# Optimization experiments

Hardware: AMD Instinct MI355X
Metric: run time of the kernel (lower is better)

Reference implementation:

```python
import jax, jax.numpy as jnp
import numpy as np

D_MODEL = 128
D_STATE = 16
D_CONV = 2
EXPAND = 2
D_INNER = EXPAND * D_MODEL  # 256
DT_RANK = (D_MODEL + 15) // 16  # 8
GROUPS = 4
EPS = 1e-5


def setup_inputs() -> dict:
    key = jax.random.key(0)
    ks = jax.random.split(key, 12)
    s = lambda k, shape, sc=0.02: jax.random.normal(k, shape, dtype=jnp.float32) * sc
    inp = {
        "x_hsi": jax.random.normal(ks[0], (8, D_MODEL, 64, 64), dtype=jnp.float32),
        "W_in": s(ks[1], (D_MODEL, 2 * D_INNER)),            # in_proj (no bias)
        "conv_w": s(ks[2], (D_INNER, D_CONV), 0.5),          # depthwise causal conv, k=2
        "conv_b": s(ks[3], (D_INNER,), 0.1),
        "W_x": s(ks[4], (D_INNER, DT_RANK + 2 * D_STATE)),   # x_proj (no bias)
        "W_dt": s(ks[5], (DT_RANK, D_INNER), 0.1),
        "b_dt": s(ks[6], (D_INNER,), 0.1),
        "A_log": jnp.log(jnp.broadcast_to(jnp.arange(1, D_STATE + 1, dtype=jnp.float32), (D_INNER, D_STATE))),
        "D": jnp.ones((D_INNER,), dtype=jnp.float32),
        "W_out": s(ks[7], (D_INNER, D_MODEL)),               # out_proj (no bias)
        "gn_gamma": jnp.ones((D_MODEL,), dtype=jnp.float32),
        "gn_beta": jnp.zeros((D_MODEL,), dtype=jnp.float32),
    }
    return inp


def _causal_conv_k2(x, w, b):
    # x: [B, L, Din]; w: [Din, 2]; causal depthwise conv, kernel size 2
    xp = jnp.pad(x, ((0, 0), (1, 0), (0, 0)))
    return xp[:, :-1] * w[:, 0] + xp[:, 1:] * w[:, 1] + b


def _selective_scan(xc, dt, Bmat, Cmat, A, D):
    # xc,dt: [B,L,Din]; Bmat,Cmat: [B,L,N]; A: [Din,N]; D: [Din]
    def step(h, inp):
        dt_t, B_t, C_t, x_t = inp          # [B,Din],[B,N],[B,N],[B,Din]
        dA = jnp.exp(dt_t[..., None] * A)                      # [B,Din,N]
        dBx = dt_t[..., None] * B_t[:, None, :] * x_t[..., None]
        h = dA * h + dBx
        y = jnp.einsum('bdn,bn->bd', h, C_t)
        return h, y

    B_, L, Din = xc.shape
    h0 = jnp.zeros((B_, Din, A.shape[1]), dtype=xc.dtype)
    xs = (jnp.swapaxes(dt, 0, 1), jnp.swapaxes(Bmat, 0, 1),
          jnp.swapaxes(Cmat, 0, 1), jnp.swapaxes(xc, 0, 1))
    _, ys = jax.lax.scan(step, h0, xs)     # ys: [L,B,Din]
    return jnp.swapaxes(ys, 0, 1) + xc * D


def _mamba(x, W_in, conv_w, conv_b, W_x, W_dt, b_dt, A_log, D, W_out):
    # x: [B, L, d_model]
    xz = x @ W_in                                   # [B,L,2*Din]
    xh, z = jnp.split(xz, 2, axis=-1)
    xh = jax.nn.silu(_causal_conv_k2(xh, conv_w, conv_b))
    x_dbl = xh @ W_x                                # [B,L,dt_rank+2N]
    dt_low = x_dbl[..., :DT_RANK]
    Bmat = x_dbl[..., DT_RANK:DT_RANK + D_STATE]
    Cmat = x_dbl[..., DT_RANK + D_STATE:]
    dt = jax.nn.softplus(dt_low @ W_dt + b_dt)      # [B,L,Din]
    A = -jnp.exp(A_log)
    y = _selective_scan(xh, dt, Bmat, Cmat, A, D)
    y = y * jax.nn.silu(z)
    return y @ W_out


def _group_norm(x, gamma, beta):
    # x: [B,C,H,W]
    B_, C, H, W = x.shape
    xr = x.reshape(B_, GROUPS, -1)
    mean = xr.mean(-1, keepdims=True)
    var = xr.var(-1, keepdims=True)
    xn = ((xr - mean) * jax.lax.rsqrt(var + EPS)).reshape(B_, C, H, W)
    return xn * gamma[:, None, None] + beta[:, None, None]


def reference(x_hsi, W_in, conv_w, conv_b, W_x, W_dt, b_dt, A_log, D, W_out, gn_gamma, gn_beta):
    B_, C, H, W = x_hsi.shape
    x = jnp.transpose(x_hsi, (0, 2, 3, 1)).reshape(B_, H * W, C)
    x = _mamba(x, W_in, conv_w, conv_b, W_x, W_dt, b_dt, A_log, D, W_out)
    x = jnp.transpose(x.reshape(B_, H, W, C), (0, 3, 1, 2))
    x = jax.nn.silu(_group_norm(x, gn_gamma, gn_beta))
    return x + x_hsi
```

## Files before the change

kernel.cpp:

```cpp
#include <hip/hip_runtime.h>
#include <hip/hip_bf16.h>
#include <hip/hip_fp16.h>
#include <math.h>

#define BATCH   8
#define LSEQ    4096
#define CMODEL  128
#define DIN     256
#define NSTATE  16
#define RRANK   8
#define NCH     128
#define TCH     32

typedef __attribute__((ext_vector_type(8))) short short8;
typedef __attribute__((ext_vector_type(4))) float f32x4;
typedef __attribute__((ext_vector_type(2))) float f32x2;

__device__ __forceinline__ float sigmoid_fast(float x) {
    return __builtin_amdgcn_rcpf(1.0f + __expf(-x));
}
__device__ __forceinline__ float silu_fast(float x) { return x * sigmoid_fast(x); }
__device__ __forceinline__ float softplus_fast(float x) {
    return fmaxf(x, 0.0f) + __logf(1.0f + __expf(-fabsf(x)));
}
__device__ __forceinline__ float bf2f(unsigned short u) {
    return __uint_as_float(((unsigned)u) << 16);
}
__device__ __forceinline__ unsigned pk2bf(float a, float b) {
    __hip_bfloat162 t = __float22bfloat162_rn(make_float2(a, b));
    unsigned r;
    __builtin_memcpy(&r, &t, 4);
    return r;
}
__device__ __forceinline__ unsigned short f2bf1(float v) {
    return (unsigned short)pk2bf(v, v);
}

__device__ __forceinline__ void dA_powers2(float dtv, const float* A, bool fast,
                                           f32x2* dA2)
{
    if (fast) {
        float e1 = __expf(dtv * A[0]);
        float e2 = e1 * e1;
        dA2[0] = (f32x2){e1, e2};
        f32x2 e2s = (f32x2){e2, e2};
        #pragma unroll
        for (int j = 1; j < 8; ++j) dA2[j] = dA2[j-1] * e2s;
    } else {
        #pragma unroll
        for (int j = 0; j < 8; ++j)
            dA2[j] = (f32x2){__expf(dtv * A[2*j]), __expf(dtv * A[2*j+1])};
    }
}

#define LSTR 72
#define YSTR 264

__device__ __forceinline__ void tr64_bf(const float* __restrict__ src, int lds,
                                        int r0, int c0,
                                        unsigned short* __restrict__ dst, int ldd)
{
    __shared__ float ts[64][65];
    const int tid = threadIdx.x;
    #pragma unroll
    for (int it = 0; it < 4; ++it) {
        int slot = tid + it * 256;
        int i = slot >> 4, j4 = slot & 15;
        float4 v = *(const float4*)&src[(size_t)(r0 + i) * lds + c0 + j4 * 4];
        ts[i][j4*4+0] = v.x; ts[i][j4*4+1] = v.y;
        ts[i][j4*4+2] = v.z; ts[i][j4*4+3] = v.w;
    }
    __syncthreads();
    #pragma unroll
    for (int it = 0; it < 4; ++it) {
        int slot = tid + it * 256;
        int row = slot >> 4, c4 = slot & 15;
        unsigned p0 = pk2bf(ts[c4*4+0][row], ts[c4*4+1][row]);
        unsigned p1 = pk2bf(ts[c4*4+2][row], ts[c4*4+3][row]);
        unsigned long long u = (unsigned long long)p0 | ((unsigned long long)p1 << 32);
        *(unsigned long long*)&dst[(size_t)(c0 + row) * ldd + r0 + c4 * 4] = u;
    }
}

__global__ __launch_bounds__(256) void k0_setup(
    const float* __restrict__ W_in, const float* __restrict__ W_out,
    unsigned short* __restrict__ wtin, unsigned short* __restrict__ wtout,
    float* __restrict__ part)
{
    const int bid = blockIdx.x;
    if (bid < 16) {
        int ct = bid >> 3, jt = bid & 7;
        tr64_bf(W_in, 512, ct * 64, jt * 64, wtin, 128);
    } else if (bid < 24) {
        int t3 = bid - 16;
        int kt = t3 >> 1, ct = t3 & 1;
        tr64_bf(W_out, 128, kt * 64, ct * 64, wtout, 256);
    } else {
        if (threadIdx.x < 64) part[threadIdx.x] = 0.0f;
    }
}

__global__ __launch_bounds__(512) void k1_gemm_in(
    const float* __restrict__ x_hsi, const unsigned short* __restrict__ wtin,
    unsigned short* __restrict__ xhbf, unsigned short* __restrict__ zbf)
{
    __shared__ __align__(16) unsigned short Abf[128 * LSTR];
    __shared__ __align__(16) unsigned short Bbf[256 * LSTR];
    const int tid = threadIdx.x;
    const int R0  = blockIdx.x * 128;
    const int b   = R0 >> 12;
    const int l0  = R0 & 4095;
    const int jbase = blockIdx.y * 256;

    const int w    = tid >> 6;
    const int lane = tid & 63;
    const int lm   = lane & 15;
    const int q    = lane >> 4;
    const int mbase = (w & 1) * 64;
    const int nbase = (w >> 1) * 64;

    f32x4 acc[4][4];
    #pragma unroll
    for (int i = 0; i < 4; ++i)
        #pragma unroll
        for (int j = 0; j < 4; ++j) acc[i][j] = (f32x4){0.f, 0.f, 0.f, 0.f};

    const int cq = tid & 15;
    const int lq = tid >> 4;

    for (int kc = 0; kc < 128; kc += 64) {
        __syncthreads();
        {
            float v[4][4];
            #pragma unroll
            for (int t = 0; t < 4; ++t) {
                float4 f = *(const float4*)&x_hsi[((b * 128 + kc + cq * 4 + t) << 12) + l0 + lq * 4];
                v[t][0] = f.x; v[t][1] = f.y; v[t][2] = f.z; v[t][3] = f.w;
            }
            #pragma unroll
            for (int i = 0; i < 4; ++i) {
                unsigned p0 = pk2bf(v[0][i], v[1][i]);
                unsigned p1 = pk2bf(v[2][i], v[3][i]);
                unsigned long long u = (unsigned long long)p0 | ((unsigned long long)p1 << 32);
                *(unsigned long long*)&Abf[(lq * 4 + i) * LSTR + cq * 4] = u;
            }
        }
        #pragma unroll
        for (int it = 0; it < 4; ++it) {
            int slot = tid + it * 512;
            int r = slot >> 3, seg = slot & 7;
            short8 vb = *(const short8*)&wtin[(size_t)(jbase + r) * 128 + kc + seg * 8];
            *(short8*)&Bbf[r * LSTR + seg * 8] = vb;
        }
        __syncthreads();
        #pragma unroll
        for (int kt = 0; kt < 2; ++kt) {
            short8 af[4], bfr[4];
            #pragma unroll
            for (int mt = 0; mt < 4; ++mt)
                af[mt] = *(const short8*)&Abf[(mbase + mt * 16 + lm) * LSTR + kt * 32 + q * 8];
            #pragma unroll
            for (int nt = 0; nt < 4; ++nt)
                bfr[nt] = *(const short8*)&Bbf[(nbase + nt * 16 + lm) * LSTR + kt * 32 + q * 8];
            #pragma unroll
            for (int mt = 0; mt < 4; ++mt)
                #pragma unroll
                for (int nt = 0; nt < 4; ++nt)
                    acc[mt][nt] = __builtin_amdgcn_mfma_f32_16x16x32_bf16(
                        af[mt], bfr[nt], acc[mt][nt], 0, 0, 0);
        }
    }

    const bool is_xh = (jbase == 0);
    #pragma unroll
    for (int mt = 0; mt < 4; ++mt) {
        #pragma unroll
        for (int r = 0; r < 4; ++r) {
            int row = R0 + mbase + mt * 16 + q * 4 + r;
            #pragma unroll
            for (int nt = 0; nt < 4; ++nt) {
                int col = nbase + nt * 16 + lm;
                float val = acc[mt][nt][r];
                if (is_xh) xhbf[row * 256 + col] = f2bf1(val);
                else       zbf[row * 256 + col]  = f2bf1(silu_fast(val));
            }
        }
    }
}

__global__ __launch_bounds__(256) void k46_conv_gemm_scan1(
    const unsigned short* __restrict__ xhbf, const float* __restrict__ conv_w,
    const float* __restrict__ conv_b, const float* __restrict__ W_x,
    const float* __restrict__ W_dt, const float* __restrict__ b_dt,
    const float* __restrict__ A_log,
    float* __restrict__ xdbl, unsigned short* __restrict__ xcbf,
    float* __restrict__ hend, float* __restrict__ dtsg)
{
    __shared__ float xcs[TCH][68];
    __shared__ __align__(16) float wxs[64 * 40];
    __shared__ float cw0[256], cw1[256], cbs[256];
    __shared__ __align__(16) unsigned short xcb[TCH][YSTR];
    const int tid = threadIdx.x;
    const int chunk = blockIdx.x;
    const int b = blockIdx.y;
    const int R0 = b * LSEQ + chunk * TCH;

    cw0[tid] = conv_w[2 * tid];
    cw1[tid] = conv_w[2 * tid + 1];
    cbs[tid] = conv_b[tid];

    const int d = tid;
    float A[16];
    #pragma unroll
    for (int qq = 0; qq < 4; ++qq) {
        float4 al = *(const float4*)&A_log[d * 16 + qq * 4];
        A[qq*4+0] = -__expf(al.x); A[qq*4+1] = -__expf(al.y);
        A[qq*4+2] = -__expf(al.z); A[qq*4+3] = -__expf(al.w);
    }
    bool fast = true;
    #pragma unroll
    for (int n = 1; n < 16; ++n)
        fast = fast && (fabsf(A[n] - (n + 1) * A[0]) <= 1e-4f * fabsf(A[n]) + 1e-7f);
    float wdt[8];
    #pragma unroll
    for (int r = 0; r < 8; ++r) wdt[r] = W_dt[r * 256 + d];
    const float bdt = b_dt[d];

    const int tc = tid & 7;
    const int tr = tid >> 3;

    float acc[5];
    #pragma unroll
    for (int j = 0; j < 5; ++j) acc[j] = 0.0f;

    for (int kc = 0; kc < 256; kc += 64) {
        __syncthreads();
        #pragma unroll
        for (int it = 0; it < 3; ++it) {
            int i4 = tid + it * 256;
            if (i4 < 640) ((float4*)wxs)[i4] = ((const float4*)&W_x[kc * 40])[i4];
        }
        #pragma unroll
        for (int it = 0; it < 2; ++it) {
            int idx = tid + it * 256;
            int r = idx >> 4, qq = idx & 15;
            int row = R0 + r;
            ushort4 cu = *(const ushort4*)&xhbf[(size_t)row * 256 + kc + qq * 4];
            float cur[4] = {bf2f(cu.x), bf2f(cu.y), bf2f(cu.z), bf2f(cu.w)};
            float pv[4] = {0.f, 0.f, 0.f, 0.f};
            if ((row & 4095) != 0) {
                ushort4 pu = *(const ushort4*)&xhbf[(size_t)(row - 1) * 256 + kc + qq * 4];
                pv[0] = bf2f(pu.x); pv[1] = bf2f(pu.y);
                pv[2] = bf2f(pu.z); pv[3] = bf2f(pu.w);
            }
            int dd = kc + qq * 4;
            float o[4];
            #pragma unroll
            for (int e = 0; e < 4; ++e)
                o[e] = silu_fast(pv[e] * cw0[dd+e] + cur[e] * cw1[dd+e] + cbs[dd+e]);
            *(float4*)&xcs[r][qq * 4] = make_float4(o[0], o[1], o[2], o[3]);
            unsigned p0 = pk2bf(o[0], o[1]), p1 = pk2bf(o[2], o[3]);
            unsigned long long u = (unsigned long long)p0 | ((unsigned long long)p1 << 32);
            *(unsigned long long*)&xcb[r][dd] = u;
            *(unsigned long long*)&xcbf[(size_t)row * 256 + dd] = u;
        }
        __syncthreads();
        #pragma unroll 2
        for (int k = 0; k < 64; ++k) {
            float wv[5];
            #pragma unroll
            for (int j = 0; j < 5; ++j) wv[j] = wxs[k * 40 + tc * 5 + j];
            float a = xcs[tr][k];
            #pragma unroll
            for (int j = 0; j < 5; ++j) acc[j] = fmaf(a, wv[j], acc[j]);
        }
    }

    __syncthreads();
    float* xdl = wxs;
    #pragma unroll
    for (int j = 0; j < 5; ++j) {
        float v = acc[j];
        xdl[tr * 40 + tc * 5 + j] = v;
        xdbl[(size_t)(R0 + tr) * 40 + tc * 5 + j] = v;
    }
    __syncthreads();

    f32x2 h2[8];
    #pragma unroll
    for (int j = 0; j < 8; ++j) h2[j] = (f32x2){0.f, 0.f};
    float dtsum = 0.f;

    #pragma unroll 2
    for (int tt = 0; tt < TCH; ++tt) {
        float xcv = bf2f(xcb[tt][d]);

        float dl[8];
        *(float4*)&dl[0] = *(const float4*)&xdl[tt * 40 + 0];
        *(float4*)&dl[4] = *(const float4*)&xdl[tt * 40 + 4];
        float dtr = bdt;
        #pragma unroll
        for (int r = 0; r < 8; ++r) dtr = fmaf(dl[r], wdt[r], dtr);
        float dtv = softplus_fast(dtr);
        dtsum += dtv;
        float dtx = dtv * xcv;

        float Bv[16];
        *(float4*)&Bv[0]  = *(const float4*)&xdl[tt * 40 + 8];
        *(float4*)&Bv[4]  = *(const float4*)&xdl[tt * 40 + 12];
        *(float4*)&Bv[8]  = *(const float4*)&xdl[tt * 40 + 16];
        *(float4*)&Bv[12] = *(const float4*)&xdl[tt * 40 + 20];

        f32x2 dA2[8];
        dA_powers2(dtv, A, fast, dA2);
        f32x2 dtx2 = (f32x2){dtx, dtx};
        #pragma unroll
        for (int j = 0; j < 8; ++j) {
            f32x2 Bt2 = (f32x2){Bv[2*j], Bv[2*j+1]};
            h2[j] = dA2[j] * h2[j] + dtx2 * Bt2;
        }
    }

    const float* hf = (const float*)h2;
    const int base = ((b * NCH + chunk) * 256 + d) * 16;
    #pragma unroll
    for (int qq = 0; qq < 4; ++qq)
        *(float4*)&hend[base + qq * 4] = make_float4(hf[qq*4], hf[qq*4+1], hf[qq*4+2], hf[qq*4+3]);
    dtsg[(b * NCH + chunk) * 256 + d] = dtsum;
}

__global__ __launch_bounds__(256) void k7_combine(
    const float* __restrict__ dtsg, const float* __restrict__ A_log,
    float* __restrict__ hx)
{
    const int idx = blockIdx.x * 256 + threadIdx.x;
    const int b = idx >> 12;
    const int rem = idx & 4095;
    const int d = rem >> 4, n = rem & 15;
    const float An = -__expf(A_log[d * 16 + n]);
    const int base = b * NCH * 4096 + rem;
    const int sbase = b * NCH * 256 + d;
    float h = 0.f;
    float Sb[8], Eb[8];
    #pragma unroll
    for (int j = 0; j < 8; ++j) {
        Sb[j] = dtsg[sbase + j * 256];
        Eb[j] = hx[base + j * 4096];
    }
    for (int g = 0; g < NCH / 8; ++g) {
        const int o  = base + g * 32768;
        const int so = sbase + g * 2048;
        float Sn[8] = {0,0,0,0,0,0,0,0}, En[8] = {0,0,0,0,0,0,0,0};
        if (g < NCH / 8 - 1) {
            #pragma unroll
            for (int j = 0; j < 8; ++j) {
                Sn[j] = dtsg[so + 2048 + j * 256];
                En[j] = hx[o + 32768 + j * 4096];
            }
        }
        #pragma unroll
        for (int j = 0; j < 8; ++j) {
            hx[o + j * 4096] = h;
            float P = __expf(Sb[j] * An);
            h = fmaf(P, h, Eb[j]);
        }
        #pragma unroll
        for (int j = 0; j < 8; ++j) { Sb[j] = Sn[j]; Eb[j] = En[j]; }
    }
}

__global__ __launch_bounds__(256) void k89_scan2_gemm_out(
    const unsigned short* __restrict__ xcbf, const float* __restrict__ xdbl,
    const float* __restrict__ W_dt, const float* __restrict__ b_dt,
    const float* __restrict__ A_log, const float* __restrict__ Dvec,
    const float* __restrict__ hin, const unsigned short* __restrict__ zbf,
    const unsigned short* __restrict__ wtout,
    unsigned short* __restrict__ out_bf, float* __restrict__ part)
{
    __shared__ __align__(16) float xdb[TCH * 40];
    __shared__ __align__(16) unsigned short Ybf[TCH][YSTR];
    __shared__ __align__(16) unsigned short Abf[128 * LSTR];
    __shared__ float pred[8];
    const int tid = threadIdx.x;
    const int chunk = blockIdx.x;
    const int b = blockIdx.y;
    const int t0 = b * LSEQ + chunk * TCH;

    #pragma unroll
    for (int it = 0; it < 2; ++it) {
        int i4 = tid + it * 256;
        if (i4 < 320) ((float4*)xdb)[i4] = ((const float4*)&xdbl[(size_t)t0 * 40])[i4];
    }
    if (tid < 8) pred[tid] = 0.0f;

    const int d = tid;
    float A[16];
    #pragma unroll
    for (int qq = 0; qq < 4; ++qq) {
        float4 al = *(const float4*)&A_log[d * 16 + qq * 4];
        A[qq*4+0] = -__expf(al.x); A[qq*4+1] = -__expf(al.y);
        A[qq*4+2] = -__expf(al.z); A[qq*4+3] = -__expf(al.w);
    }
    bool fast = true;
    #pragma unroll
    for (int n = 1; n < 16; ++n)
        fast = fast && (fabsf(A[n] - (n + 1) * A[0]) <= 1e-4f * fabsf(A[n]) + 1e-7f);
    float wdt[8];
    #pragma unroll
    for (int r = 0; r < 8; ++r) wdt[r] = W_dt[r * 256 + d];
    const float bdt = b_dt[d];
    const float Dd = Dvec[d];

    f32x2 h2[8];
    {
        const int hbase = ((b * NCH + chunk) * 256 + d) * 16;
        float hf[16];
        #pragma unroll
        for (int qq = 0; qq < 4; ++qq) {
            float4 hv = *(const float4*)&hin[hbase + qq * 4];
            hf[qq*4+0] = hv.x; hf[qq*4+1] = hv.y; hf[qq*4+2] = hv.z; hf[qq*4+3] = hv.w;
        }
        #pragma unroll
        for (int j = 0; j < 8; ++j) h2[j] = (f32x2){hf[2*j], hf[2*j+1]};
    }
    __syncthreads();

    #pragma unroll 2
    for (int tt = 0; tt < TCH; ++tt) {
        const size_t gi = (size_t)(t0 + tt) * 256 + d;
        float xcv = bf2f(xcbf[gi]);

        float dl[8];
        *(float4*)&dl[0] = *(const float4*)&xdb[tt * 40 + 0];
        *(float4*)&dl[4] = *(const float4*)&xdb[tt * 40 + 4];
        float dtr = bdt;
        #pragma unroll
        for (int r = 0; r < 8; ++r) dtr = fmaf(dl[r], wdt[r], dtr);
        float dtv = softplus_fast(dtr);
        float dtx = dtv * xcv;

        float Bv[16], Cv[16];
        *(float4*)&Bv[0]  = *(const float4*)&xdb[tt * 40 + 8];
        *(float4*)&Bv[4]  = *(const float4*)&xdb[tt * 40 + 12];
        *(float4*)&Bv[8]  = *(const float4*)&xdb[tt * 40 + 16];
        *(float4*)&Bv[12] = *(const float4*)&xdb[tt * 40 + 20];
        *(float4*)&Cv[0]  = *(const float4*)&xdb[tt * 40 + 24];
        *(float4*)&Cv[4]  = *(const float4*)&xdb[tt * 40 + 28];
        *(float4*)&Cv[8]  = *(const float4*)&xdb[tt * 40 + 32];
        *(float4*)&Cv[12] = *(const float4*)&xdb[tt * 40 + 36];

        f32x2 dA2[8];
        dA_powers2(dtv, A, fast, dA2);
        f32x2 dtx2 = (f32x2){dtx, dtx};
        f32x2 yv2 = (f32x2){0.f, 0.f};
        #pragma unroll
        for (int j = 0; j < 8; ++j) {
            f32x2 Bt2 = (f32x2){Bv[2*j], Bv[2*j+1]};
            f32x2 Ct2 = (f32x2){Cv[2*j], Cv[2*j+1]};
            h2[j] = dA2[j] * h2[j] + dtx2 * Bt2;
            yv2 = yv2 + h2[j] * Ct2;
        }
        float yv = yv2.x + yv2.y;
        yv = fmaf(Dd, xcv, yv);
        Ybf[tt][d] = f2bf1(yv * bf2f(zbf[gi]));
    }

    const int w    = tid >> 6;
    const int lane = tid & 63;
    const int lm   = lane & 15;
    const int q    = lane >> 4;
    const int mbase = (w & 1) * 64;
    const int nbase = (w >> 1) * 16;

    f32x4 acc[4];
    #pragma unroll
    for (int i = 0; i < 4; ++i) acc[i] = (f32x4){0.f, 0.f, 0.f, 0.f};

    for (int kc = 0; kc < 256; kc += 64) {
        __syncthreads();
        #pragma unroll
        for (int it = 0; it < 4; ++it) {
            int slot = tid + it * 256;
            int r = slot >> 3, seg = slot & 7;
            short8 va = *(const short8*)&wtout[(size_t)r * 256 + kc + seg * 8];
            *(short8*)&Abf[r * LSTR + seg * 8] = va;
        }
        __syncthreads();
        #pragma unroll
        for (int kt = 0; kt < 2; ++kt) {
            short8 af[4], bfr;
            #pragma unroll
            for (int mt = 0; mt < 4; ++mt)
                af[mt] = *(const short8*)&Abf[(mbase + mt * 16 + lm) * LSTR + kt * 32 + q * 8];
            bfr = *(const short8*)&Ybf[nbase + lm][kc + kt * 32 + q * 8];
            #pragma unroll
            for (int mt = 0; mt < 4; ++mt)
                acc[mt] = __builtin_amdgcn_mfma_f32_16x16x32_bf16(
                    af[mt], bfr, acc[mt], 0, 0, 0);
        }
    }

    const int l0 = chunk * TCH;
    #pragma unroll
    for (int mt = 0; mt < 4; ++mt) {
        #pragma unroll
        for (int r = 0; r < 4; ++r) {
            int c = mbase + mt * 16 + q * 4 + r;
            long obase = (long)(b * 128 + c) * 4096 + l0;
            out_bf[obase + nbase + lm] = f2bf1(acc[mt][r]);
        }
    }

    float s0 = 0.f, q0 = 0.f, s1 = 0.f, q1 = 0.f;
    #pragma unroll
    for (int mt = 0; mt < 4; ++mt)
        #pragma unroll
        for (int r = 0; r < 4; ++r) {
            float v = acc[mt][r];
            if (mt < 2) { s0 += v; q0 += v * v; }
            else        { s1 += v; q1 += v * v; }
        }
    #pragma unroll
    for (int off = 32; off > 0; off >>= 1) {
        s0 += __shfl_down(s0, off, 64);
        q0 += __shfl_down(q0, off, 64);
        s1 += __shfl_down(s1, off, 64);
        q1 += __shfl_down(q1, off, 64);
    }
    if (lane == 0) {
        int g0 = mbase >> 5;
        atomicAdd(&pred[g0 * 2],           s0);
        atomicAdd(&pred[g0 * 2 + 1],       q0);
        atomicAdd(&pred[(g0 + 1) * 2],     s1);
        atomicAdd(&pred[(g0 + 1) * 2 + 1], q1);
    }
    __syncthreads();
    if (tid < 8) atomicAdd(&part[b * 8 + tid], pred[tid]);
}

__global__ __launch_bounds__(256) void k10c_apply(
    const unsigned short* __restrict__ out_bf, const float* __restrict__ part,
    const float* __restrict__ gamma, const float* __restrict__ beta,
    const float* __restrict__ x_hsi, float* __restrict__ out)
{
    __shared__ float sstat[64];
    if (threadIdx.x < 32) {
        float S = part[threadIdx.x * 2];
        float Q = part[threadIdx.x * 2 + 1];
        const float inv_n = 1.0f / 131072.0f;
        float mean = S * inv_n;
        float var  = Q * inv_n - mean * mean;
        sstat[threadIdx.x * 2]     = mean;
        sstat[threadIdx.x * 2 + 1] = rsqrtf(var + 1e-5f);
    }
    __syncthreads();
    const int idx4 = blockIdx.x * 256 + threadIdx.x;
    const int flat = idx4 * 4;
    const int c = (flat >> 12) & 127;
    const int b = flat >> 19;
    const int g = c >> 5;
    const float mean = sstat[(b * 4 + g) * 2];
    const float inv  = sstat[(b * 4 + g) * 2 + 1];
    const float ga = gamma[c], be = beta[c];
    ushort4 u = *(const ushort4*)&out_bf[flat];
    float4 r = *(const float4*)&x_hsi[flat];
    float vv[4] = {bf2f(u.x), bf2f(u.y), bf2f(u.z), bf2f(u.w)};
    float rr[4] = {r.x, r.y, r.z, r.w};
    float o[4];
    #pragma unroll
    for (int qq = 0; qq < 4; ++qq) {
        float xn = (vv[qq] - mean) * inv;
        float gv = xn * ga + be;
        o[qq] = silu_fast(gv) + rr[qq];
    }
    *(float4*)&out[flat] = make_float4(o[0], o[1], o[2], o[3]);
}

extern "C" void kernel_launch(void* const* d_in, const int* in_sizes, int n_in,
                              void* d_out, int out_size, void* d_ws, size_t ws_size,
                              hipStream_t stream)
{
    const float* x_hsi  = (const float*)d_in[0];
    const float* W_in   = (const float*)d_in[1];
    const float* conv_w = (const float*)d_in[2];
    const float* conv_b = (const float*)d_in[3];
    const float* W_x    = (const float*)d_in[4];
    const float* W_dt   = (const float*)d_in[5];
    const float* b_dt   = (const float*)d_in[6];
    const float* A_log  = (const float*)d_in[7];
    const float* Dv     = (const float*)d_in[8];
    const float* W_out  = (const float*)d_in[9];
    const float* gnw    = (const float*)d_in[10];
    const float* gnb    = (const float*)d_in[11];

    float* ws = (float*)d_ws;
    unsigned short* xhbf = (unsigned short*)(ws + 0);
    unsigned short* zbf  = (unsigned short*)(ws + 4194304);
    float* xdbl   = ws + 8388608;
    float* hx     = ws + 8716288;
    float* dtsg   = ws + 12910592;
    unsigned short* xcbf   = (unsigned short*)(ws + 13172736);
    unsigned short* out_bf = (unsigned short*)(ws + 17367040);
    float* part   = ws + 19464192;
    unsigned short* wtin  = (unsigned short*)(ws + 19464256);
    unsigned short* wtout = (unsigned short*)(ws + 19497024);
    float* outp   = (float*)d_out;

    k0_setup<<<25, 256, 0, stream>>>(W_in, W_out, wtin, wtout, part);
    k1_gemm_in<<<dim3(256, 2), 512, 0, stream>>>(x_hsi, wtin, xhbf, zbf);
    k46_conv_gemm_scan1<<<dim3(NCH, BATCH), 256, 0, stream>>>(
        xhbf, conv_w, conv_b, W_x, W_dt, b_dt, A_log, xdbl, xcbf, hx, dtsg);
    k7_combine<<<128, 256, 0, stream>>>(dtsg, A_log, hx);
    k89_scan2_gemm_out<<<dim3(NCH, BATCH), 256, 0, stream>>>(
        xcbf, xdbl, W_dt, b_dt, A_log, Dv, hx, zbf, wtout, out_bf, part);
    k10c_apply<<<4096, 256, 0, stream>>>(out_bf, part, gnw, gnb, x_hsi, outp);
}
```

Before: 195.1 us.

## Use MFMA for x_proj GEMM and read weight fragments directly from global

The small x_proj GEMM in the conv/scan kernel moves from scalar FP32 FMAs to bf16 MFMA, using a transposed, padded bf16 copy of W_x built once in the setup kernel. In the input and output GEMMs, the LDS staging of the weight tiles is dropped and B/A fragments are loaded straight from global or L2. This removes LDS traffic, barriers and shared memory per block, which may raise occupancy. The cost is more global loads per wave and reduced precision in x_proj, whose outputs feed dt, B and C.

```diff
diff --git a/kernel.cpp b/kernel.cpp
--- a/kernel.cpp
+++ b/kernel.cpp
@@ -84,8 +84,9 @@
 
 __global__ __launch_bounds__(256) void k0_setup(
     const float* __restrict__ W_in, const float* __restrict__ W_out,
+    const float* __restrict__ W_x,
     unsigned short* __restrict__ wtin, unsigned short* __restrict__ wtout,
-    float* __restrict__ part)
+    unsigned short* __restrict__ wxt, float* __restrict__ part)
 {
     const int bid = blockIdx.x;
     if (bid < 16) {
@@ -95,6 +96,12 @@
         int t3 = bid - 16;
         int kt = t3 >> 1, ct = t3 & 1;
         tr64_bf(W_out, 128, kt * 64, ct * 64, wtout, 256);
+    } else if (bid == 24) {
+        for (int idx = threadIdx.x; idx < 48 * 256; idx += 256) {
+            int j = idx >> 8, k = idx & 255;
+            float v = (j < 40) ? W_x[k * 40 + j] : 0.0f;
+            wxt[(size_t)j * 256 + k] = f2bf1(v);
+        }
     } else {
         if (threadIdx.x < 64) part[threadIdx.x] = 0.0f;
     }
@@ -105,7 +112,6 @@
     unsigned short* __restrict__ xhbf, unsigned short* __restrict__ zbf)
 {
     __shared__ __align__(16) unsigned short Abf[128 * LSTR];
-    __shared__ __align__(16) unsigned short Bbf[256 * LSTR];
     const int tid = threadIdx.x;
     const int R0  = blockIdx.x * 128;
     const int b   = R0 >> 12;
@@ -145,13 +151,6 @@
                 *(unsigned long long*)&Abf[(lq * 4 + i) * LSTR + cq * 4] = u;
             }
         }
-        #pragma unroll
-        for (int it = 0; it < 4; ++it) {
-            int slot = tid + it * 512;
-            int r = slot >> 3, seg = slot & 7;
-            short8 vb = *(const short8*)&wtin[(size_t)(jbase + r) * 128 + kc + seg * 8];
-            *(short8*)&Bbf[r * LSTR + seg * 8] = vb;
-        }
         __syncthreads();
         #pragma unroll
         for (int kt = 0; kt < 2; ++kt) {
@@ -161,7 +160,7 @@
                 af[mt] = *(const short8*)&Abf[(mbase + mt * 16 + lm) * LSTR + kt * 32 + q * 8];
             #pragma unroll
             for (int nt = 0; nt < 4; ++nt)
-                bfr[nt] = *(const short8*)&Bbf[(nbase + nt * 16 + lm) * LSTR + kt * 32 + q * 8];
+                bfr[nt] = *(const short8*)&wtin[(size_t)(jbase + nbase + nt * 16 + lm) * 128 + kc + kt * 32 + q * 8];
             #pragma unroll
             for (int mt = 0; mt < 4; ++mt)
                 #pragma unroll
@@ -190,16 +189,15 @@
 
 __global__ __launch_bounds__(256) void k46_conv_gemm_scan1(
     const unsigned short* __restrict__ xhbf, const float* __restrict__ conv_w,
-    const float* __restrict__ conv_b, const float* __restrict__ W_x,
+    const float* __restrict__ conv_b, const unsigned short* __restrict__ wxt,
     const float* __restrict__ W_dt, const float* __restrict__ b_dt,
     const float* __restrict__ A_log,
     float* __restrict__ xdbl, unsigned short* __restrict__ xcbf,
     float* __restrict__ hend, float* __restrict__ dtsg)
 {
-    __shared__ float xcs[TCH][68];
-    __shared__ __align__(16) float wxs[64 * 40];
     __shared__ float cw0[256], cw1[256], cbs[256];
     __shared__ __align__(16) unsigned short xcb[TCH][YSTR];
+    __shared__ __align__(16) float xdl[TCH * 40];
     const int tid = threadIdx.x;
     const int chunk = blockIdx.x;
     const int b = blockIdx.y;
@@ -226,63 +224,70 @@
     for (int r = 0; r < 8; ++r) wdt[r] = W_dt[r * 256 + d];
     const float bdt = b_dt[d];
 
-    const int tc = tid & 7;
-    const int tr = tid >> 3;
-
-    float acc[5];
-    #pragma unroll
-    for (int j = 0; j < 5; ++j) acc[j] = 0.0f;
-
-    for (int kc = 0; kc < 256; kc += 64) {
-        __syncthreads();
-        #pragma unroll
-        for (int it = 0; it < 3; ++it) {
-            int i4 = tid + it * 256;
-            if (i4 < 640) ((float4*)wxs)[i4] = ((const float4*)&W_x[kc * 40])[i4];
-        }
-        #pragma unroll
-        for (int it = 0; it < 2; ++it) {
-            int idx = tid + it * 256;
-            int r = idx >> 4, qq = idx & 15;
-            int row = R0 + r;
-            ushort4 cu = *(const ushort4*)&xhbf[(size_t)row * 256 + kc + qq * 4];
-            float cur[4] = {bf2f(cu.x), bf2f(cu.y), bf2f(cu.z), bf2f(cu.w)};
-            float pv[4] = {0.f, 0.f, 0.f, 0.f};
-            if ((row & 4095) != 0) {
-                ushort4 pu = *(const ushort4*)&xhbf[(size_t)(row - 1) * 256 + kc + qq * 4];
-                pv[0] = bf2f(pu.x); pv[1] = bf2f(pu.y);
-                pv[2] = bf2f(pu.z); pv[3] = bf2f(pu.w);
+    __syncthreads();
+
+    #pragma unroll
+    for (int it = 0; it < 8; ++it) {
+        int idx = tid + it * 256;
+        int r = idx >> 6, qq = idx & 63;
+        int row = R0 + r;
+        int dd = qq * 4;
+        ushort4 cu = *(const ushort4*)&xhbf[(size_t)row * 256 + dd];
+        float cur[4] = {bf2f(cu.x), bf2f(cu.y), bf2f(cu.z), bf2f(cu.w)};
+        float pv[4] = {0.f, 0.f, 0.f, 0.f};
+        if ((row & 4095) != 0) {
+            ushort4 pu = *(const ushort4*)&xhbf[(size_t)(row - 1) * 256 + dd];
+            pv[0] = bf2f(pu.x); pv[1] = bf2f(pu.y);
+            pv[2] = bf2f(pu.z); pv[3] = bf2f(pu.w);
+        }
+        float o[4];
+        #pragma unroll
+        for (int e = 0; e < 4; ++e)
+            o[e] = silu_fast(pv[e] * cw0[dd+e] + cur[e] * cw1[dd+e] + cbs[dd+e]);
+        unsigned p0 = pk2bf(o[0], o[1]), p1 = pk2bf(o[2], o[3]);
+        unsigned long long u = (unsigned long long)p0 | ((unsigned long long)p1 << 32);
+        *(unsigned long long*)&xcb[r][dd] = u;
+        *(unsigned long long*)&xcbf[(size_t)row * 256 + dd] = u;
+    }
+    __syncthreads();
+
+    const int w    = tid >> 6;
+    const int lane = tid & 63;
+    const int lm   = lane & 15;
+    const int q    = lane >> 4;
+    {
+        const int mt  = w & 1;
+        const int nlo = (w < 2) ? 0 : 2;
+        const int nn  = (w < 2) ? 2 : 1;
+        f32x4 macc[2];
+        macc[0] = (f32x4){0.f,0.f,0.f,0.f};
+        macc[1] = (f32x4){0.f,0.f,0.f,0.f};
+        for (int kc = 0; kc < 256; kc += 32) {
+            short8 af = *(const short8*)&xcb[mt * 16 + lm][kc + q * 8];
+            #pragma unroll
+            for (int t = 0; t < 2; ++t) {
+                if (t < nn) {
+                    short8 bfr = *(const short8*)&wxt[(size_t)((nlo + t) * 16 + lm) * 256 + kc + q * 8];
+                    macc[t] = __builtin_amdgcn_mfma_f32_16x16x32_bf16(
+                        af, bfr, macc[t], 0, 0, 0);
+                }
             }
-            int dd = kc + qq * 4;
-            float o[4];
-            #pragma unroll
-            for (int e = 0; e < 4; ++e)
-                o[e] = silu_fast(pv[e] * cw0[dd+e] + cur[e] * cw1[dd+e] + cbs[dd+e]);
-            *(float4*)&xcs[r][qq * 4] = make_float4(o[0], o[1], o[2], o[3]);
-            unsigned p0 = pk2bf(o[0], o[1]), p1 = pk2bf(o[2], o[3]);
-            unsigned long long u = (unsigned long long)p0 | ((unsigned long long)p1 << 32);
-            *(unsigned long long*)&xcb[r][dd] = u;
-            *(unsigned long long*)&xcbf[(size_t)row * 256 + dd] = u;
-        }
-        __syncthreads();
-        #pragma unroll 2
-        for (int k = 0; k < 64; ++k) {
-            float wv[5];
-            #pragma unroll
-            for (int j = 0; j < 5; ++j) wv[j] = wxs[k * 40 + tc * 5 + j];
-            float a = xcs[tr][k];
-            #pragma unroll
-            for (int j = 0; j < 5; ++j) acc[j] = fmaf(a, wv[j], acc[j]);
-        }
-    }
-
-    __syncthreads();
-    float* xdl = wxs;
-    #pragma unroll
-    for (int j = 0; j < 5; ++j) {
-        float v = acc[j];
-        xdl[tr * 40 + tc * 5 + j] = v;
-        xdbl[(size_t)(R0 + tr) * 40 + tc * 5 + j] = v;
+        }
+        #pragma unroll
+        for (int t = 0; t < 2; ++t) {
+            if (t < nn) {
+                #pragma unroll
+                for (int r = 0; r < 4; ++r) {
+                    int row = mt * 16 + q * 4 + r;
+                    int col = (nlo + t) * 16 + lm;
+                    if (col < 40) {
+                        float v = macc[t][r];
+                        xdl[row * 40 + col] = v;
+                        xdbl[(size_t)(R0 + row) * 40 + col] = v;
+                    }
+                }
+            }
+        }
     }
     __syncthreads();
 
@@ -379,7 +384,6 @@
 {
     __shared__ __align__(16) float xdb[TCH * 40];
     __shared__ __align__(16) unsigned short Ybf[TCH][YSTR];
-    __shared__ __align__(16) unsigned short Abf[128 * LSTR];
     __shared__ float pred[8];
     const int tid = threadIdx.x;
     const int chunk = blockIdx.x;
@@ -464,6 +468,7 @@
         yv = fmaf(Dd, xcv, yv);
         Ybf[tt][d] = f2bf1(yv * bf2f(zbf[gi]));
     }
+    __syncthreads();
 
     const int w    = tid >> 6;
     const int lane = tid & 63;
@@ -476,27 +481,13 @@
     #pragma unroll
     for (int i = 0; i < 4; ++i) acc[i] = (f32x4){0.f, 0.f, 0.f, 0.f};
 
-    for (int kc = 0; kc < 256; kc += 64) {
-        __syncthreads();
-        #pragma unroll
-        for (int it = 0; it < 4; ++it) {
-            int slot = tid + it * 256;
-            int r = slot >> 3, seg = slot & 7;
-            short8 va = *(const short8*)&wtout[(size_t)r * 256 + kc + seg * 8];
-            *(short8*)&Abf[r * LSTR + seg * 8] = va;
-        }
-        __syncthreads();
-        #pragma unroll
-        for (int kt = 0; kt < 2; ++kt) {
-            short8 af[4], bfr;
-            #pragma unroll
-            for (int mt = 0; mt < 4; ++mt)
-                af[mt] = *(const short8*)&Abf[(mbase + mt * 16 + lm) * LSTR + kt * 32 + q * 8];
-            bfr = *(const short8*)&Ybf[nbase + lm][kc + kt * 32 + q * 8];
-            #pragma unroll
-            for (int mt = 0; mt < 4; ++mt)
-                acc[mt] = __builtin_amdgcn_mfma_f32_16x16x32_bf16(
-                    af[mt], bfr, acc[mt], 0, 0, 0);
+    for (int ks = 0; ks < 256; ks += 32) {
+        short8 bfr = *(const short8*)&Ybf[nbase + lm][ks + q * 8];
+        #pragma unroll
+        for (int mt = 0; mt < 4; ++mt) {
+            short8 af = *(const short8*)&wtout[(size_t)(mbase + mt * 16 + lm) * 256 + ks + q * 8];
+            acc[mt] = __builtin_amdgcn_mfma_f32_16x16x32_bf16(
+                af, bfr, acc[mt], 0, 0, 0);
         }
     }
 
@@ -604,12 +595,13 @@
     float* part   = ws + 19464192;
     unsigned short* wtin  = (unsigned short*)(ws + 19464256);
     unsigned short* wtout = (unsigned short*)(ws + 19497024);
+    unsigned short* wxt   = (unsigned short*)(ws + 19513408);
     float* outp   = (float*)d_out;
 
-    k0_setup<<<25, 256, 0, stream>>>(W_in, W_out, wtin, wtout, part);
+    k0_setup<<<26, 256, 0, stream>>>(W_in, W_out, W_x, wtin, wtout, wxt, part);
     k1_gemm_in<<<dim3(256, 2), 512, 0, stream>>>(x_hsi, wtin, xhbf, zbf);
     k46_conv_gemm_scan1<<<dim3(NCH, BATCH), 256, 0, stream>>>(
-        xhbf, conv_w, conv_b, W_x, W_dt, b_dt, A_log, xdbl, xcbf, hx, dtsg);
+        xhbf, conv_w, conv_b, wxt, W_dt, b_dt, A_log, xdbl, xcbf, hx, dtsg);
     k7_combine<<<128, 256, 0, stream>>>(dtsg, A_log, hx);
     k89_scan2_gemm_out<<<dim3(NCH, BATCH), 256, 0, stream>>>(
         xcbf, xdbl, W_dt, b_dt, A_log, Dv, hx, zbf, wtout, out_bf, part);
```

Result: slower. 200.1 us (+2.5%).
